# Optimization experiments

Hardware: AMD Instinct MI355X
Metric: run time of the kernel (lower is better)

## Reference

```python
import jax, jax.numpy as jnp
import numpy as np

HIDDEN = 1024
HEADS = 16
HEAD = HIDDEN // HEADS


def setup_inputs() -> dict:
    key = jax.random.key(0)
    ks = jax.random.split(key, 10)
    s = 1.0 / np.sqrt(HIDDEN)
    inp = {
        "x": jax.random.normal(ks[0], (2, 2048, HIDDEN), dtype=jnp.float32),
        "Wq": jax.random.uniform(ks[1], (HIDDEN, HIDDEN), jnp.float32, -s, s),
        "bq": jnp.zeros((HIDDEN,), jnp.float32),
        "Wk": jax.random.uniform(ks[2], (HIDDEN, HIDDEN), jnp.float32, -s, s),
        "bk": jnp.zeros((HIDDEN,), jnp.float32),
        "Wv": jax.random.uniform(ks[3], (HIDDEN, HIDDEN), jnp.float32, -s, s),
        "bv": jnp.zeros((HIDDEN,), jnp.float32),
        "Wo": jax.random.uniform(ks[4], (HIDDEN, HIDDEN), jnp.float32, -s, s),
        "bo": jnp.zeros((HIDDEN,), jnp.float32),
        "ln_g": jnp.ones((HIDDEN,), jnp.float32),
        "ln_b": jnp.zeros((HIDDEN,), jnp.float32),
    }
    return inp


def reference(x, Wq, bq, Wk, bk, Wv, bv, Wo, bo, ln_g, ln_b):
    B, S, H = x.shape
    # pre-LN (eps=1e-5 like torch LayerNorm)
    mu = jnp.mean(x, axis=-1, keepdims=True)
    var = jnp.mean(jnp.square(x - mu), axis=-1, keepdims=True)
    xn = (x - mu) * jax.lax.rsqrt(var + 1e-5) * ln_g + ln_b
    # QKV projections (torch Linear: x @ W.T + b) -> [B,S,heads,head]
    q = (xn @ Wq.T + bq).reshape(B, S, HEADS, HEAD)
    k = (xn @ Wk.T + bk).reshape(B, S, HEADS, HEAD)
    v = (xn @ Wv.T + bv).reshape(B, S, HEADS, HEAD)
    # scaled dot-product attention, naive full scores [B,heads,S,S]
    scores = jnp.einsum("bqhd,bkhd->bhqk", q, k) / jnp.sqrt(jnp.float32(HEAD))
    attn = jax.nn.softmax(scores, axis=-1)
    ctx = jnp.einsum("bhqk,bkhd->bqhd", attn, v).reshape(B, S, H)
    out = ctx @ Wo.T + bo
    return x + out  # dropout is identity in eval
```

## Files before the change

kernel.cpp:

```cpp
#include <hip/hip_runtime.h>
#include <hip/hip_bf16.h>
#include <stdint.h>

#define HID 1024
#define SEQ 2048
#define BATCH 2
#define NHEADS 16
#define HEADDIM 64
#define MROWS (BATCH*SEQ)

#define GAS __attribute__((address_space(1)))
#define LAS __attribute__((address_space(3)))

typedef __attribute__((ext_vector_type(8))) __bf16 bf16x8;
typedef __attribute__((ext_vector_type(4))) float f32x4;
typedef __attribute__((ext_vector_type(2))) uint32_t u32x2;

__device__ __forceinline__ ushort f2bf(float f) {
  union { float f; uint32_t u; } v; v.f = f;
  return (ushort)((v.u + 0x7FFFu + ((v.u >> 16) & 1u)) >> 16);
}

__device__ __forceinline__ void gl_lds16(const void* g, void* l) {
  __builtin_amdgcn_global_load_lds((const GAS void*)g, (LAS void*)l, 16, 0, 0);
}

__global__ __launch_bounds__(256) void k_cvt(const float* __restrict__ Wq,
                                             const float* __restrict__ Wk,
                                             const float* __restrict__ Wv,
                                             const float* __restrict__ Wo,
                                             ushort* __restrict__ dst) {
  int mat = blockIdx.y;
  const float* src = (mat == 0) ? Wq : (mat == 1) ? Wk : (mat == 2) ? Wv : Wo;
  int off = (blockIdx.x * 256 + threadIdx.x) * 4;
  float4 v = *(const float4*)(src + off);
  ushort4 o;
  o.x = f2bf(v.x); o.y = f2bf(v.y); o.z = f2bf(v.z); o.w = f2bf(v.w);
  *(ushort4*)(dst + (size_t)mat * (HID * HID) + off) = o;
}

__global__ __launch_bounds__(256) void k_ln(const float* __restrict__ x,
                                            const float* __restrict__ g,
                                            const float* __restrict__ b,
                                            ushort* __restrict__ xn) {
  int row = blockIdx.x;
  int t = threadIdx.x;
  const float* xr = x + (size_t)row * HID;
  float4 v = *(const float4*)(xr + t * 4);
  float s = v.x + v.y + v.z + v.w;
  float s2 = v.x * v.x + v.y * v.y + v.z * v.z + v.w * v.w;
  for (int m = 1; m < 64; m <<= 1) { s += __shfl_xor(s, m); s2 += __shfl_xor(s2, m); }
  __shared__ float ws[4], ws2[4];
  int wid = t >> 6;
  if ((t & 63) == 0) { ws[wid] = s; ws2[wid] = s2; }
  __syncthreads();
  s = ws[0] + ws[1] + ws[2] + ws[3];
  s2 = ws2[0] + ws2[1] + ws2[2] + ws2[3];
  float mu = s * (1.0f / HID);
  float var = s2 * (1.0f / HID) - mu * mu;
  float rstd = rsqrtf(var + 1e-5f);
  float4 gg = *(const float4*)(g + t * 4);
  float4 bb = *(const float4*)(b + t * 4);
  ushort4 o;
  o.x = f2bf((v.x - mu) * rstd * gg.x + bb.x);
  o.y = f2bf((v.y - mu) * rstd * gg.y + bb.y);
  o.z = f2bf((v.z - mu) * rstd * gg.z + bb.z);
  o.w = f2bf((v.w - mu) * rstd * gg.w + bb.w);
  *(ushort4*)(xn + (size_t)row * HID + t * 4) = o;
}

__global__ __launch_bounds__(256) void k_qkv(const ushort* __restrict__ xn,
                                             const ushort* __restrict__ wmat,
                                             const float* __restrict__ bq,
                                             const float* __restrict__ bk,
                                             const float* __restrict__ bv,
                                             ushort* __restrict__ qo,
                                             ushort* __restrict__ ko,
                                             ushort* __restrict__ vo) {
  __shared__ ushort As[128 * 32];
  __shared__ ushort Bs[128 * 32];
  int tid = threadIdx.x;
  int lane = tid & 63;
  int wv = tid >> 6;
  int quad = lane >> 4;
  int l16 = lane & 15;
  int m0 = blockIdx.x * 128;
  int ng = blockIdx.y * 128;
  int mat = ng >> 10;
  int nloc = ng & 1023;
  const ushort* wptr = wmat + (size_t)mat * (HID * HID) + (size_t)nloc * HID;
  const float* bias = (mat == 0) ? bq : (mat == 1) ? bk : bv;
  ushort* outp = (mat == 0) ? qo : (mat == 1) ? ko : vo;
  const float scl = (mat == 0) ? 0.18033688011112042f : 1.0f;

  int arow = tid >> 2;
  int acol = (tid & 3) * 8;
  int wm = (wv >> 1) * 64, wn = (wv & 1) * 64;

  f32x4 acc[4][4] = {};
  for (int k0 = 0; k0 < HID; k0 += 32) {
    __syncthreads();
    for (int t = 0; t < 2; t++) {
      gl_lds16(xn + (size_t)(m0 + t * 64 + arow) * HID + k0 + acol,
               As + t * 2048 + wv * 512);
      gl_lds16(wptr + (size_t)(t * 64 + arow) * HID + k0 + acol,
               Bs + t * 2048 + wv * 512);
    }
    __syncthreads();
    bf16x8 af[4], bfr[4];
    for (int i = 0; i < 4; i++)
      af[i] = *(const bf16x8*)&As[(wm + i * 16 + l16) * 32 + quad * 8];
    for (int n = 0; n < 4; n++)
      bfr[n] = *(const bf16x8*)&Bs[(wn + n * 16 + l16) * 32 + quad * 8];
    for (int i = 0; i < 4; i++)
      for (int n = 0; n < 4; n++)
        acc[i][n] = __builtin_amdgcn_mfma_f32_16x16x32_bf16(af[i], bfr[n], acc[i][n], 0, 0, 0);
  }
  float bv4[4];
  for (int n = 0; n < 4; n++) bv4[n] = bias[nloc + wn + n * 16 + l16];
  for (int i = 0; i < 4; i++) {
    int mrow = m0 + wm + i * 16 + quad * 4;
    for (int n = 0; n < 4; n++) {
      int col = nloc + wn + n * 16 + l16;
      int h = col >> 6, d = col & 63;
      for (int r = 0; r < 4; r++) {
        int m = mrow + r;
        int bidx = m >> 11, sidx = m & 2047;
        size_t dst;
        if (mat == 2)
          dst = (((size_t)(bidx * NHEADS + h) * HEADDIM) + d) * SEQ + sidx;
        else
          dst = (((size_t)(bidx * NHEADS + h) * SEQ) + sidx) * HEADDIM + d;
        outp[dst] = f2bf((acc[i][n][r] + bv4[n]) * scl);
      }
    }
  }
}

__global__ __launch_bounds__(256, 4) void k_attn(const ushort* __restrict__ Q,
                                                 const ushort* __restrict__ K,
                                                 const ushort* __restrict__ Vt,
                                                 ushort* __restrict__ ctx) {
  __shared__ ushort Ksm[2][64 * 64];
  __shared__ ushort Vsm[2][64 * 64];
  __shared__ ushort Psm[4][16 * 64];
  int tid = threadIdx.x, lane = tid & 63, wv = tid >> 6, quad = lane >> 4, l16 = lane & 15;
  int bh = blockIdx.y;
  int q0 = blockIdx.x * 64;
  const ushort* Qb = Q + ((size_t)bh * SEQ + q0 + wv * 16) * HEADDIM;
  const ushort* Kb = K + (size_t)bh * SEQ * HEADDIM;
  const ushort* Vb = Vt + (size_t)bh * HEADDIM * SEQ;
  ushort* Pw = Psm[wv];

  bf16x8 qf[2];
  for (int c = 0; c < 2; c++)
    qf[c] = *(const bf16x8*)(Qb + (size_t)l16 * HEADDIM + c * 32 + quad * 8);

  bf16x8 ones;
  for (int j = 0; j < 8; j++) ones[j] = (__bf16)1.0f;

  int gsl = lane & 7;
  int rowA = wv * 8 + (lane >> 3);
  int rowB = 32 + wv * 8 + (lane >> 3);
  const ushort* kSrcA = Kb + rowA * HEADDIM + ((gsl ^ ((rowA >> 2) & 7)) * 8);
  const ushort* kSrcB = Kb + rowB * HEADDIM + ((gsl ^ ((rowB >> 2) & 7)) * 8);
  const ushort* vSrcA = Vb + (size_t)rowA * SEQ + ((gsl ^ (rowA & 7)) * 8);
  const ushort* vSrcB = Vb + (size_t)rowB * SEQ + ((gsl ^ (rowB & 7)) * 8);
  int ldsA = wv * 512;
  int ldsB = 2048 + wv * 512;

  f32x4 Oa[4] = {};
  f32x4 Os = {};
  int fk = l16 & 7;

  gl_lds16(kSrcA, &Ksm[0][ldsA]);
  gl_lds16(kSrcB, &Ksm[0][ldsB]);
  gl_lds16(vSrcA, &Vsm[0][ldsA]);
  gl_lds16(vSrcB, &Vsm[0][ldsB]);
  __syncthreads();

  for (int kt = 0; kt < SEQ / 64; kt++) {
    int buf = kt & 1;
    if (kt + 1 < SEQ / 64) {
      int nb = buf ^ 1;
      size_t ko = (size_t)(kt + 1) * 64 * HEADDIM;
      size_t vo = (size_t)(kt + 1) * 64;
      gl_lds16(kSrcA + ko, &Ksm[nb][ldsA]);
      gl_lds16(kSrcB + ko, &Ksm[nb][ldsB]);
      gl_lds16(vSrcA + vo, &Vsm[nb][ldsA]);
      gl_lds16(vSrcB + vo, &Vsm[nb][ldsB]);
    }

    f32x4 sacc[4] = {};
    for (int nt = 0; nt < 4; nt++) {
      int krow = 4 * l16 + nt;
      for (int c = 0; c < 2; c++) {
        int kb = c * 4 + quad;
        bf16x8 kf = *(const bf16x8*)&Ksm[buf][krow * 64 + ((kb ^ fk) * 8)];
        sacc[nt] = __builtin_amdgcn_mfma_f32_16x16x32_bf16(qf[c], kf, sacc[nt], 0, 0, 0);
      }
    }

    for (int r = 0; r < 4; r++) {
      union { float f; uint32_t u; } p0, p1, p2, p3;
      p0.f = __builtin_amdgcn_exp2f(fminf(sacc[0][r], 80.f));
      p1.f = __builtin_amdgcn_exp2f(fminf(sacc[1][r], 80.f));
      p2.f = __builtin_amdgcn_exp2f(fminf(sacc[2][r], 80.f));
      p3.f = __builtin_amdgcn_exp2f(fminf(sacc[3][r], 80.f));
      uint32_t pk01 = __builtin_amdgcn_perm(p1.u, p0.u, 0x07060302u);
      uint32_t pk23 = __builtin_amdgcn_perm(p3.u, p2.u, 0x07060302u);
      int row = quad * 4 + r;
      int idx = (row * 8 + ((l16 >> 1) ^ (row & 7))) * 8 + (l16 & 1) * 4;
      *(u32x2*)&Pw[idx] = (u32x2){pk01, pk23};
    }

    for (int c = 0; c < 2; c++) {
      int kb = c * 4 + quad;
      bf16x8 pf0 = *(const bf16x8*)&Pw[(l16 * 8 + (kb ^ fk)) * 8];
      Os = __builtin_amdgcn_mfma_f32_16x16x32_bf16(pf0, ones, Os, 0, 0, 0);
      for (int nt = 0; nt < 4; nt++) {
        int d = nt * 16 + l16;
        bf16x8 vf = *(const bf16x8*)&Vsm[buf][d * 64 + ((kb ^ fk) * 8)];
        Oa[nt] = __builtin_amdgcn_mfma_f32_16x16x32_bf16(pf0, vf, Oa[nt], 0, 0, 0);
      }
    }
    __syncthreads();
  }

  int bidx = bh >> 4, h = bh & 15;
  for (int r = 0; r < 4; r++) {
    float inv = 1.0f / Os[r];
    int sidx = q0 + wv * 16 + quad * 4 + r;
    size_t base = ((size_t)(bidx * SEQ) + sidx) * HID + h * HEADDIM;
    for (int nt = 0; nt < 4; nt++)
      ctx[base + nt * 16 + l16] = f2bf(Oa[nt][r] * inv);
  }
}

__global__ __launch_bounds__(256) void k_oproj(const ushort* __restrict__ ctx,
                                               const ushort* __restrict__ wmat,
                                               const float* __restrict__ bo,
                                               const float* __restrict__ x,
                                               float* __restrict__ out) {
  __shared__ ushort As[128 * 32];
  __shared__ ushort Bs[128 * 32];
  int tid = threadIdx.x;
  int lane = tid & 63;
  int wv = tid >> 6;
  int quad = lane >> 4;
  int l16 = lane & 15;
  int m0 = blockIdx.x * 128;
  int n0 = blockIdx.y * 128;
  const ushort* wptr = wmat + (size_t)3 * (HID * HID) + (size_t)n0 * HID;
  int arow = tid >> 2;
  int acol = (tid & 3) * 8;
  int wm = (wv >> 1) * 64, wn = (wv & 1) * 64;

  f32x4 acc[4][4] = {};
  for (int k0 = 0; k0 < HID; k0 += 32) {
    __syncthreads();
    for (int t = 0; t < 2; t++) {
      gl_lds16(ctx + (size_t)(m0 + t * 64 + arow) * HID + k0 + acol,
               As + t * 2048 + wv * 512);
      gl_lds16(wptr + (size_t)(t * 64 + arow) * HID + k0 + acol,
               Bs + t * 2048 + wv * 512);
    }
    __syncthreads();
    bf16x8 af[4], bfr[4];
    for (int i = 0; i < 4; i++)
      af[i] = *(const bf16x8*)&As[(wm + i * 16 + l16) * 32 + quad * 8];
    for (int n = 0; n < 4; n++)
      bfr[n] = *(const bf16x8*)&Bs[(wn + n * 16 + l16) * 32 + quad * 8];
    for (int i = 0; i < 4; i++)
      for (int n = 0; n < 4; n++)
        acc[i][n] = __builtin_amdgcn_mfma_f32_16x16x32_bf16(af[i], bfr[n], acc[i][n], 0, 0, 0);
  }
  float bv4[4];
  for (int n = 0; n < 4; n++) bv4[n] = bo[n0 + wn + n * 16 + l16];
  for (int i = 0; i < 4; i++) {
    int mrow = m0 + wm + i * 16 + quad * 4;
    for (int n = 0; n < 4; n++) {
      int col = n0 + wn + n * 16 + l16;
      for (int r = 0; r < 4; r++) {
        size_t idx = (size_t)(mrow + r) * HID + col;
        out[idx] = acc[i][n][r] + bv4[n] + x[idx];
      }
    }
  }
}

extern "C" void kernel_launch(void* const* d_in, const int* in_sizes, int n_in,
                              void* d_out, int out_size, void* d_ws, size_t ws_size,
                              hipStream_t stream) {
  const float* x    = (const float*)d_in[0];
  const float* Wq   = (const float*)d_in[1];
  const float* bq   = (const float*)d_in[2];
  const float* Wk   = (const float*)d_in[3];
  const float* bk   = (const float*)d_in[4];
  const float* Wv   = (const float*)d_in[5];
  const float* bv   = (const float*)d_in[6];
  const float* Wo   = (const float*)d_in[7];
  const float* bo   = (const float*)d_in[8];
  const float* ln_g = (const float*)d_in[9];
  const float* ln_b = (const float*)d_in[10];
  float* out = (float*)d_out;

  const size_t MB = 1024 * 1024;
  ushort* ws_w = (ushort*)d_ws;
  ushort* xn   = (ushort*)((char*)d_ws + 8 * MB);
  ushort* Qw   = (ushort*)((char*)d_ws + 16 * MB);
  ushort* Kw   = (ushort*)((char*)d_ws + 24 * MB);
  ushort* Vw   = (ushort*)((char*)d_ws + 32 * MB);
  ushort* Cw   = (ushort*)((char*)d_ws + 40 * MB);

  k_cvt<<<dim3(1024, 4), 256, 0, stream>>>(Wq, Wk, Wv, Wo, ws_w);
  k_ln<<<dim3(MROWS), 256, 0, stream>>>(x, ln_g, ln_b, xn);
  k_qkv<<<dim3(32, 24), 256, 0, stream>>>(xn, ws_w, bq, bk, bv, Qw, Kw, Vw);
  k_attn<<<dim3(SEQ / 64, BATCH * NHEADS), 256, 0, stream>>>(Qw, Kw, Vw, Cw);
  k_oproj<<<dim3(32, 8), 256, 0, stream>>>(Cw, ws_w, bo, x, out);
}
```

Measured before the change: 213.9 us.

## Rewrite attention with 32x32x16 MFMA and register-resident P via permlane swaps

The attention kernel moves from 16x16x32 to 32x32x16 bf16 MFMA and computes S transposed (K as the A operand), with 32 query rows per wave and 128 rows per block. P is now packed with v_cvt_pk_bf16_f32 and rearranged in registers with v_permlane32_swap, so the per-wave LDS staging buffer and its writes and reads go away. The K swizzle is changed to match the new access pattern, and s_setprio brackets the MFMA phases. Fewer blocks run with more registers each (launch bounds lowered to 2), which risks lower occupancy and less latency hiding, and the gfx950-specific inline asm depends on the exact lane layout being right.

```diff
diff --git a/kernel.cpp b/kernel.cpp
--- a/kernel.cpp
+++ b/kernel.cpp
@@ -14,7 +14,7 @@
 
 typedef __attribute__((ext_vector_type(8))) __bf16 bf16x8;
 typedef __attribute__((ext_vector_type(4))) float f32x4;
-typedef __attribute__((ext_vector_type(2))) uint32_t u32x2;
+typedef __attribute__((ext_vector_type(16))) float f32x16;
 
 __device__ __forceinline__ ushort f2bf(float f) {
   union { float f; uint32_t u; } v; v.f = f;
@@ -23,6 +23,16 @@
 
 __device__ __forceinline__ void gl_lds16(const void* g, void* l) {
   __builtin_amdgcn_global_load_lds((const GAS void*)g, (LAS void*)l, 16, 0, 0);
+}
+
+__device__ __forceinline__ uint32_t cvtpk(float a, float b) {
+  uint32_t r;
+  asm("v_cvt_pk_bf16_f32 %0, %1, %2" : "=v"(r) : "v"(a), "v"(b));
+  return r;
+}
+
+__device__ __forceinline__ void pl32swap(uint32_t& a, uint32_t& b) {
+  asm("v_permlane32_swap_b32 %0, %1" : "+v"(a), "+v"(b));
 }
 
 __global__ __launch_bounds__(256) void k_cvt(const float* __restrict__ Wq,
@@ -137,41 +147,41 @@
   }
 }
 
-__global__ __launch_bounds__(256, 4) void k_attn(const ushort* __restrict__ Q,
+__global__ __launch_bounds__(256, 2) void k_attn(const ushort* __restrict__ Q,
                                                  const ushort* __restrict__ K,
                                                  const ushort* __restrict__ Vt,
                                                  ushort* __restrict__ ctx) {
   __shared__ ushort Ksm[2][64 * 64];
   __shared__ ushort Vsm[2][64 * 64];
-  __shared__ ushort Psm[4][16 * 64];
-  int tid = threadIdx.x, lane = tid & 63, wv = tid >> 6, quad = lane >> 4, l16 = lane & 15;
+  int tid = threadIdx.x, lane = tid & 63, wv = tid >> 6;
+  int l32 = lane & 31, hi = lane >> 5;
   int bh = blockIdx.y;
-  int q0 = blockIdx.x * 64;
-  const ushort* Qb = Q + ((size_t)bh * SEQ + q0 + wv * 16) * HEADDIM;
+  int q0 = blockIdx.x * 128;
+  const ushort* Qb = Q + ((size_t)bh * SEQ + q0 + wv * 32 + l32) * HEADDIM;
   const ushort* Kb = K + (size_t)bh * SEQ * HEADDIM;
   const ushort* Vb = Vt + (size_t)bh * HEADDIM * SEQ;
-  ushort* Pw = Psm[wv];
-
-  bf16x8 qf[2];
-  for (int c = 0; c < 2; c++)
-    qf[c] = *(const bf16x8*)(Qb + (size_t)l16 * HEADDIM + c * 32 + quad * 8);
+
+  bf16x8 qf[4];
+#pragma unroll
+  for (int f = 0; f < 4; f++)
+    qf[f] = *(const bf16x8*)(Qb + f * 16 + hi * 8);
 
   bf16x8 ones;
+#pragma unroll
   for (int j = 0; j < 8; j++) ones[j] = (__bf16)1.0f;
 
   int gsl = lane & 7;
   int rowA = wv * 8 + (lane >> 3);
   int rowB = 32 + wv * 8 + (lane >> 3);
-  const ushort* kSrcA = Kb + rowA * HEADDIM + ((gsl ^ ((rowA >> 2) & 7)) * 8);
-  const ushort* kSrcB = Kb + rowB * HEADDIM + ((gsl ^ ((rowB >> 2) & 7)) * 8);
+  const ushort* kSrcA = Kb + rowA * HEADDIM + ((gsl ^ (rowA & 7)) * 8);
+  const ushort* kSrcB = Kb + rowB * HEADDIM + ((gsl ^ (rowB & 7)) * 8);
   const ushort* vSrcA = Vb + (size_t)rowA * SEQ + ((gsl ^ (rowA & 7)) * 8);
   const ushort* vSrcB = Vb + (size_t)rowB * SEQ + ((gsl ^ (rowB & 7)) * 8);
   int ldsA = wv * 512;
   int ldsB = 2048 + wv * 512;
 
-  f32x4 Oa[4] = {};
-  f32x4 Os = {};
-  int fk = l16 & 7;
+  f32x16 Oa0 = {}, Oa1 = {}, Os = {};
+  int rsw = (l32 & 7);
 
   gl_lds16(kSrcA, &Ksm[0][ldsA]);
   gl_lds16(kSrcB, &Ksm[0][ldsB]);
@@ -191,49 +201,87 @@
       gl_lds16(vSrcB + vo, &Vsm[nb][ldsB]);
     }
 
-    f32x4 sacc[4] = {};
-    for (int nt = 0; nt < 4; nt++) {
-      int krow = 4 * l16 + nt;
-      for (int c = 0; c < 2; c++) {
-        int kb = c * 4 + quad;
-        bf16x8 kf = *(const bf16x8*)&Ksm[buf][krow * 64 + ((kb ^ fk) * 8)];
-        sacc[nt] = __builtin_amdgcn_mfma_f32_16x16x32_bf16(qf[c], kf, sacc[nt], 0, 0, 0);
-      }
-    }
-
-    for (int r = 0; r < 4; r++) {
-      union { float f; uint32_t u; } p0, p1, p2, p3;
-      p0.f = __builtin_amdgcn_exp2f(fminf(sacc[0][r], 80.f));
-      p1.f = __builtin_amdgcn_exp2f(fminf(sacc[1][r], 80.f));
-      p2.f = __builtin_amdgcn_exp2f(fminf(sacc[2][r], 80.f));
-      p3.f = __builtin_amdgcn_exp2f(fminf(sacc[3][r], 80.f));
-      uint32_t pk01 = __builtin_amdgcn_perm(p1.u, p0.u, 0x07060302u);
-      uint32_t pk23 = __builtin_amdgcn_perm(p3.u, p2.u, 0x07060302u);
-      int row = quad * 4 + r;
-      int idx = (row * 8 + ((l16 >> 1) ^ (row & 7))) * 8 + (l16 & 1) * 4;
-      *(u32x2*)&Pw[idx] = (u32x2){pk01, pk23};
-    }
-
-    for (int c = 0; c < 2; c++) {
-      int kb = c * 4 + quad;
-      bf16x8 pf0 = *(const bf16x8*)&Pw[(l16 * 8 + (kb ^ fk)) * 8];
-      Os = __builtin_amdgcn_mfma_f32_16x16x32_bf16(pf0, ones, Os, 0, 0, 0);
-      for (int nt = 0; nt < 4; nt++) {
-        int d = nt * 16 + l16;
-        bf16x8 vf = *(const bf16x8*)&Vsm[buf][d * 64 + ((kb ^ fk) * 8)];
-        Oa[nt] = __builtin_amdgcn_mfma_f32_16x16x32_bf16(pf0, vf, Oa[nt], 0, 0, 0);
-      }
-    }
+    f32x16 s0 = {}, s1 = {};
+    __builtin_amdgcn_s_setprio(1);
+#pragma unroll
+    for (int f = 0; f < 4; f++) {
+      int g = 2 * f + hi;
+      bf16x8 k0 = *(const bf16x8*)&Ksm[buf][l32 * 64 + ((g ^ rsw) * 8)];
+      bf16x8 k1 = *(const bf16x8*)&Ksm[buf][(32 + l32) * 64 + ((g ^ rsw) * 8)];
+      s0 = __builtin_amdgcn_mfma_f32_32x32x16_bf16(k0, qf[f], s0, 0, 0, 0);
+      s1 = __builtin_amdgcn_mfma_f32_32x32x16_bf16(k1, qf[f], s1, 0, 0, 0);
+    }
+    __builtin_amdgcn_s_setprio(0);
+
+    union { uint32_t u[4]; bf16x8 v; } pf0, pf1, pf2, pf3;
+    {
+      uint32_t c0 = cvtpk(__builtin_amdgcn_exp2f(fminf(s0[0], 80.f)),
+                          __builtin_amdgcn_exp2f(fminf(s0[1], 80.f)));
+      uint32_t c1 = cvtpk(__builtin_amdgcn_exp2f(fminf(s0[2], 80.f)),
+                          __builtin_amdgcn_exp2f(fminf(s0[3], 80.f)));
+      uint32_t c2 = cvtpk(__builtin_amdgcn_exp2f(fminf(s0[4], 80.f)),
+                          __builtin_amdgcn_exp2f(fminf(s0[5], 80.f)));
+      uint32_t c3 = cvtpk(__builtin_amdgcn_exp2f(fminf(s0[6], 80.f)),
+                          __builtin_amdgcn_exp2f(fminf(s0[7], 80.f)));
+      uint32_t c4 = cvtpk(__builtin_amdgcn_exp2f(fminf(s0[8], 80.f)),
+                          __builtin_amdgcn_exp2f(fminf(s0[9], 80.f)));
+      uint32_t c5 = cvtpk(__builtin_amdgcn_exp2f(fminf(s0[10], 80.f)),
+                          __builtin_amdgcn_exp2f(fminf(s0[11], 80.f)));
+      uint32_t c6 = cvtpk(__builtin_amdgcn_exp2f(fminf(s0[12], 80.f)),
+                          __builtin_amdgcn_exp2f(fminf(s0[13], 80.f)));
+      uint32_t c7 = cvtpk(__builtin_amdgcn_exp2f(fminf(s0[14], 80.f)),
+                          __builtin_amdgcn_exp2f(fminf(s0[15], 80.f)));
+      pl32swap(c0, c2); pl32swap(c1, c3); pl32swap(c4, c6); pl32swap(c5, c7);
+      pf0.u[0] = c0; pf0.u[1] = c1; pf0.u[2] = c2; pf0.u[3] = c3;
+      pf1.u[0] = c4; pf1.u[1] = c5; pf1.u[2] = c6; pf1.u[3] = c7;
+    }
+    {
+      uint32_t c0 = cvtpk(__builtin_amdgcn_exp2f(fminf(s1[0], 80.f)),
+                          __builtin_amdgcn_exp2f(fminf(s1[1], 80.f)));
+      uint32_t c1 = cvtpk(__builtin_amdgcn_exp2f(fminf(s1[2], 80.f)),
+                          __builtin_amdgcn_exp2f(fminf(s1[3], 80.f)));
+      uint32_t c2 = cvtpk(__builtin_amdgcn_exp2f(fminf(s1[4], 80.f)),
+                          __builtin_amdgcn_exp2f(fminf(s1[5], 80.f)));
+      uint32_t c3 = cvtpk(__builtin_amdgcn_exp2f(fminf(s1[6], 80.f)),
+                          __builtin_amdgcn_exp2f(fminf(s1[7], 80.f)));
+      uint32_t c4 = cvtpk(__builtin_amdgcn_exp2f(fminf(s1[8], 80.f)),
+                          __builtin_amdgcn_exp2f(fminf(s1[9], 80.f)));
+      uint32_t c5 = cvtpk(__builtin_amdgcn_exp2f(fminf(s1[10], 80.f)),
+                          __builtin_amdgcn_exp2f(fminf(s1[11], 80.f)));
+      uint32_t c6 = cvtpk(__builtin_amdgcn_exp2f(fminf(s1[12], 80.f)),
+                          __builtin_amdgcn_exp2f(fminf(s1[13], 80.f)));
+      uint32_t c7 = cvtpk(__builtin_amdgcn_exp2f(fminf(s1[14], 80.f)),
+                          __builtin_amdgcn_exp2f(fminf(s1[15], 80.f)));
+      pl32swap(c0, c2); pl32swap(c1, c3); pl32swap(c4, c6); pl32swap(c5, c7);
+      pf2.u[0] = c0; pf2.u[1] = c1; pf2.u[2] = c2; pf2.u[3] = c3;
+      pf3.u[0] = c4; pf3.u[1] = c5; pf3.u[2] = c6; pf3.u[3] = c7;
+    }
+
+    __builtin_amdgcn_s_setprio(1);
+#pragma unroll
+    for (int kf = 0; kf < 4; kf++) {
+      int g = 2 * kf + hi;
+      bf16x8 pv = (kf == 0) ? pf0.v : (kf == 1) ? pf1.v : (kf == 2) ? pf2.v : pf3.v;
+      bf16x8 v0 = *(const bf16x8*)&Vsm[buf][l32 * 64 + ((g ^ rsw) * 8)];
+      bf16x8 v1 = *(const bf16x8*)&Vsm[buf][(32 + l32) * 64 + ((g ^ rsw) * 8)];
+      Oa0 = __builtin_amdgcn_mfma_f32_32x32x16_bf16(pv, v0, Oa0, 0, 0, 0);
+      Oa1 = __builtin_amdgcn_mfma_f32_32x32x16_bf16(pv, v1, Oa1, 0, 0, 0);
+      Os  = __builtin_amdgcn_mfma_f32_32x32x16_bf16(pv, ones, Os, 0, 0, 0);
+    }
+    __builtin_amdgcn_s_setprio(0);
+
     __syncthreads();
   }
 
   int bidx = bh >> 4, h = bh & 15;
-  for (int r = 0; r < 4; r++) {
+#pragma unroll
+  for (int r = 0; r < 16; r++) {
     float inv = 1.0f / Os[r];
-    int sidx = q0 + wv * 16 + quad * 4 + r;
+    int qloc = (r & 3) + 8 * (r >> 2) + 4 * hi;
+    int sidx = q0 + wv * 32 + qloc;
     size_t base = ((size_t)(bidx * SEQ) + sidx) * HID + h * HEADDIM;
-    for (int nt = 0; nt < 4; nt++)
-      ctx[base + nt * 16 + l16] = f2bf(Oa[nt][r] * inv);
+    ctx[base + l32]      = f2bf(Oa0[r] * inv);
+    ctx[base + 32 + l32] = f2bf(Oa1[r] * inv);
   }
 }
 
@@ -316,6 +364,6 @@
   k_cvt<<<dim3(1024, 4), 256, 0, stream>>>(Wq, Wk, Wv, Wo, ws_w);
   k_ln<<<dim3(MROWS), 256, 0, stream>>>(x, ln_g, ln_b, xn);
   k_qkv<<<dim3(32, 24), 256, 0, stream>>>(xn, ws_w, bq, bk, bv, Qw, Kw, Vw);
-  k_attn<<<dim3(SEQ / 64, BATCH * NHEADS), 256, 0, stream>>>(Qw, Kw, Vw, Cw);
+  k_attn<<<dim3(SEQ / 128, BATCH * NHEADS), 256, 0, stream>>>(Qw, Kw, Vw, Cw);
   k_oproj<<<dim3(32, 8), 256, 0, stream>>>(Cw, ws_w, bo, x, out);
 }
```

Measured after the change: 208.3 us. 2.7% less time.
